# Kernel tuning notes

Measured on AMD Instinct MI355X. Metric: run time of the kernel, lower is better.

Reference implementation:

```python
import jax, jax.numpy as jnp
import numpy as np

B, S, D, H = 2, 2048, 1024, 16
HD = D // H

def setup_inputs() -> dict:
    key = jax.random.key(0)
    ks = jax.random.split(key, 7)
    s = 1.0 / np.sqrt(D)
    return {
        "x": jax.random.normal(ks[0], (B, S, D), dtype=jnp.float32),
        "Wq": jax.random.uniform(ks[1], (D, D), jnp.float32, -s, s),
        "bq": jax.random.uniform(ks[2], (D,), jnp.float32, -s, s),
        "Wk": jax.random.uniform(ks[3], (D, D), jnp.float32, -s, s),
        "bk": jax.random.uniform(ks[4], (D,), jnp.float32, -s, s),
        "Wv": jax.random.uniform(ks[5], (D, D), jnp.float32, -s, s),
        "bv": jax.random.uniform(ks[6], (D,), jnp.float32, -s, s),
    }

def reference(x, Wq, bq, Wk, bk, Wv, bv):
    b, s, d = x.shape
    def proj(W, bias):
        # [b,s,d] -> [b,H,s,hd]
        y = x @ W + bias
        return y.reshape(b, s, H, HD).transpose(0, 2, 1, 3)
    Q = proj(Wq, bq)
    K = proj(Wk, bk)
    V = proj(Wv, bv)
    # NOTE: original scales by head_dim**0.5 (not sqrt) -> divide by sqrt(HD)
    scores = jnp.einsum("bhqd,bhkd->bhqk", Q, K) / (HD ** 0.5)
    attn = jax.nn.softmax(scores, axis=-1)
    out = jnp.einsum("bhqk,bhkd->bhqd", attn, V)
    out = out.transpose(0, 2, 1, 3).reshape(b, s, d)
    return out + x
```

## Files before the change

### kernel.cpp

```cpp
#include <hip/hip_runtime.h>
#include <stdint.h>

typedef float f32x4 __attribute__((ext_vector_type(4)));
typedef __bf16 bf16x8 __attribute__((ext_vector_type(8)));

union Frag {
    bf16x8 v;
    uint32_t u[4];
    __bf16 e[8];
    uint4 q;
};

constexpr int B_ = 2, S_ = 2048, D_ = 1024, H_ = 16, HD_ = 64;
constexpr int M_ = B_ * S_;

__host__ __device__ constexpr int kperm(int kl) {
    return ((kl & 12) << 1) | ((kl & 16) >> 2) | (kl & 3);
}

typedef const __attribute__((address_space(1))) char gch_t;
typedef __attribute__((address_space(3))) char lch_t;
#define GLD(g, l) __builtin_amdgcn_global_load_lds((gch_t*)(g), (lch_t*)(l), 16, 0, 0)

#define MFMA16(a, b, c) __builtin_amdgcn_mfma_f32_16x16x32_bf16((a), (b), (c), 0, 0, 0)

#define WAIT5 do { asm volatile("s_waitcnt vmcnt(5)" ::: "memory"); \
                   __builtin_amdgcn_sched_barrier(0); } while (0)
#define WAIT2 do { asm volatile("s_waitcnt vmcnt(2)" ::: "memory"); \
                   __builtin_amdgcn_sched_barrier(0); } while (0)
#define WAIT0 do { asm volatile("s_waitcnt vmcnt(0)" ::: "memory"); \
                   __builtin_amdgcn_sched_barrier(0); } while (0)
#define BARR() __builtin_amdgcn_s_barrier()

__global__ __launch_bounds__(256) void k_prep(
        const float* __restrict__ x, const float* __restrict__ Wq,
        const float* __restrict__ Wk, const float* __restrict__ Wv,
        __bf16* __restrict__ xb, __bf16* __restrict__ Wt) {
    __shared__ float tile[32][33];
    const int tid = threadIdx.x;

    if (blockIdx.x < 512) {
        int t = blockIdx.x * 256 + tid;
        const float4* src = (const float4*)(x + (size_t)t * 32);
        __bf16 buf[32];
#pragma unroll
        for (int j = 0; j < 8; ++j) {
            float4 f = src[j];
            buf[kperm(4 * j + 0)] = (__bf16)f.x;
            buf[kperm(4 * j + 1)] = (__bf16)f.y;
            buf[kperm(4 * j + 2)] = (__bf16)f.z;
            buf[kperm(4 * j + 3)] = (__bf16)f.w;
        }
        uint4* dst = (uint4*)(xb + (size_t)t * 32);
#pragma unroll
        for (int j = 0; j < 4; ++j) dst[j] = ((const uint4*)buf)[j];
        return;
    }

    int pb = blockIdx.x - 512;
    int p = pb >> 10;
    int rem = pb & 1023;
    const float* W = (p == 0) ? Wq : (p == 1 ? Wk : Wv);
    int n0 = (rem & 31) * 32, k0 = (rem >> 5) * 32;
    int tx = tid & 31, ty = tid >> 5;
#pragma unroll
    for (int t = 0; t < 4; ++t)
        tile[ty + 8 * t][tx] = W[(size_t)(k0 + ty + 8 * t) * D_ + n0 + tx];
    __syncthreads();
#pragma unroll
    for (int t = 0; t < 4; ++t)
        Wt[(size_t)(p * D_ + n0 + ty + 8 * t) * D_ + k0 + kperm(tx)] = (__bf16)tile[tx][ty + 8 * t];
}

__global__ __launch_bounds__(512, 4) void k_qkv(
        const __bf16* __restrict__ xb, const __bf16* __restrict__ Wt,
        const float* __restrict__ bq, const float* __restrict__ bk, const float* __restrict__ bv,
        __bf16* __restrict__ Qb, __bf16* __restrict__ Kb, __bf16* __restrict__ Vt) {
    __shared__ __align__(16) char ldsA[2][16384];
    __shared__ __align__(16) char ldsB[2][24576];

    const int tid = threadIdx.x;
    const int lane = tid & 63, wid = tid >> 6;
    const int wr = wid >> 2, wc = wid & 3;
    const int g = lane >> 4, qr = lane & 15, qr7 = qr & 7;
    const int lr = lane >> 3, lp = lane & 7;
    const int c = lp ^ lr;

    int bid = blockIdx.x;
    int xcd = bid & 7, local = bid >> 3;
    int mt = (xcd & 3) * 8 + (local & 7);
    int nt = (xcd >> 2) * 8 + (local >> 3);
    const int m0 = mt * 128, n0 = nt * 192;

    const __bf16* aSrc = xb + (size_t)(m0 + wid * 16 + lr) * D_ + c * 8;
    const __bf16* bSrc = Wt + (size_t)(n0 + wid * 24 + lr) * D_ + c * 8;
    const int dstA = wid * 2048;
    const int dstB = wid * 3072;

    f32x4 acc[4][3] = {};

    auto STAGE = [&](int buf, int kk) {
        GLD(aSrc + kk,           ldsA[buf] + dstA);
        GLD(aSrc + kk + 8 * D_,  ldsA[buf] + dstA + 1024);
        GLD(bSrc + kk,           ldsB[buf] + dstB);
        GLD(bSrc + kk + 8 * D_,  ldsB[buf] + dstB + 1024);
        GLD(bSrc + kk + 16 * D_, ldsB[buf] + dstB + 2048);
    };
    auto COMPUTE = [&](int buf) {
#pragma unroll
        for (int kc = 0; kc < 2; ++kc) {
            Frag afr[4], bfr[3];
#pragma unroll
            for (int mi = 0; mi < 4; ++mi) {
                int r = wr * 64 + mi * 16 + qr;
                afr[mi].q = *(const uint4*)(ldsA[buf] + r * 128 + (((4 * kc + g) ^ qr7) << 4));
            }
#pragma unroll
            for (int ni = 0; ni < 3; ++ni) {
                int r = wc * 48 + ni * 16 + qr;
                bfr[ni].q = *(const uint4*)(ldsB[buf] + r * 128 + (((4 * kc + g) ^ qr7) << 4));
            }
            __builtin_amdgcn_s_setprio(1);
#pragma unroll
            for (int mi = 0; mi < 4; ++mi)
#pragma unroll
                for (int ni = 0; ni < 3; ++ni)
                    acc[mi][ni] = MFMA16(afr[mi].v, bfr[ni].v, acc[mi][ni]);
            __builtin_amdgcn_s_setprio(0);
        }
    };

    STAGE(0, 0);
    STAGE(1, 64);
    for (int t = 0; t < 12; t += 2) {
        WAIT5; BARR(); COMPUTE(0); BARR(); STAGE(0, (t + 2) * 64);
        WAIT5; BARR(); COMPUTE(1); BARR(); STAGE(1, (t + 3) * 64);
    }
    WAIT5; BARR(); COMPUTE(0); BARR(); STAGE(0, 14 * 64);
    WAIT5; BARR(); COMPUTE(1); BARR(); STAGE(1, 15 * 64);
    WAIT5; BARR(); COMPUTE(0);
    WAIT0; BARR(); COMPUTE(1);

#pragma unroll
    for (int ni = 0; ni < 3; ++ni) {
        int n = n0 + wc * 48 + ni * 16 + qr;
        int p = n >> 10;
        int d = n & 1023;
        const float* bias = (p == 0) ? bq : (p == 1 ? bk : bv);
        float bb = bias[d];
        int h = d >> 6, hd = d & 63;
        int hd_s = (hd & 32) | kperm(hd & 31);
#pragma unroll
        for (int mi = 0; mi < 4; ++mi) {
#pragma unroll
            for (int r = 0; r < 4; ++r) {
                int m = m0 + wr * 64 + mi * 16 + 4 * g + r;
                float vv = acc[mi][ni][r] + bb;
                int b = m >> 11, s = m & 2047;
                if (p == 0) {
                    vv *= 0.18033688f;
                    Qb[((size_t)((b * H_ + h) * S_ + s)) * HD_ + hd_s] = (__bf16)vv;
                } else if (p == 1) {
                    Kb[((size_t)((b * H_ + h) * S_ + s)) * HD_ + hd_s] = (__bf16)vv;
                } else {
                    int s_s = (s & ~31) | kperm(s & 31);
                    Vt[((size_t)((b * H_ + h) * HD_ + hd)) * S_ + s_s] = (__bf16)vv;
                }
            }
        }
    }
}

__global__ __launch_bounds__(512) void k_attn(
        const __bf16* __restrict__ Qb, const __bf16* __restrict__ Kb,
        const __bf16* __restrict__ Vt, const float* __restrict__ x,
        float* __restrict__ out) {
    __shared__ __align__(16) char ldsK[2][8192];
    __shared__ __align__(16) char ldsV[2][8192];

    const int tid = threadIdx.x;
    const int lane = tid & 63, w = tid >> 6;
    const int g = lane >> 4, qr = lane & 15, qr7 = qr & 7;
    const int lr = lane >> 3, lp = lane & 7;
    const int c = lp ^ lr;

    int lid = blockIdx.x;
    int xcd = lid & 7, loc = lid >> 3;
    int bh = xcd * 4 + (loc >> 4);
    int q0 = (loc & 15) * 128;
    const int qrow = q0 + w * 16 + qr;

    Frag qf[2];
    const __bf16* qp = Qb + ((size_t)bh * S_ + qrow) * HD_;
    qf[0].q = *(const uint4*)(qp + g * 8);
    qf[1].q = *(const uint4*)(qp + 32 + g * 8);

    const __bf16* kSrc = Kb + ((size_t)bh * S_ + w * 8 + lr) * HD_ + c * 8;
    const __bf16* vSrc = Vt + ((size_t)bh * HD_ + w * 8 + lr) * S_ + c * 8;
    const int dstOff = w * 8 * 128;

    f32x4 oacc[4] = {};
    f32x4 lacc = {};

    Frag ones;
    ones.u[0] = ones.u[1] = ones.u[2] = ones.u[3] = 0x3f803f80u;

    auto STAGE = [&](int buf, int kv0) {
        GLD(kSrc + (size_t)kv0 * HD_, ldsK[buf] + dstOff);
        GLD(vSrc + kv0,               ldsV[buf] + dstOff);
    };

    auto TILE = [&](int buf) {
        f32x4 sc[4];
        __builtin_amdgcn_s_setprio(1);
#pragma unroll
        for (int kt = 0; kt < 4; ++kt) {
            const char* base = ldsK[buf] + (kt * 16 + qr) * 128;
            Frag k0, k1;
            k0.q = *(const uint4*)(base + ((g ^ qr7) << 4));
            k1.q = *(const uint4*)(base + (((4 + g) ^ qr7) << 4));
            f32x4 z = {};
            z = MFMA16(k0.v, qf[0].v, z);
            z = MFMA16(k1.v, qf[1].v, z);
            sc[kt] = z;
        }
        __builtin_amdgcn_s_setprio(0);

        Frag pa[2];
#pragma unroll
        for (int r = 0; r < 4; ++r) {
            pa[0].e[r]     = (__bf16)__builtin_amdgcn_exp2f(sc[0][r]);
            pa[0].e[4 + r] = (__bf16)__builtin_amdgcn_exp2f(sc[1][r]);
            pa[1].e[r]     = (__bf16)__builtin_amdgcn_exp2f(sc[2][r]);
            pa[1].e[4 + r] = (__bf16)__builtin_amdgcn_exp2f(sc[3][r]);
        }

        __builtin_amdgcn_s_setprio(1);
        lacc = MFMA16(pa[0].v, ones.v, lacc);
        lacc = MFMA16(pa[1].v, ones.v, lacc);

#pragma unroll
        for (int ni = 0; ni < 4; ++ni) {
            const char* base = ldsV[buf] + (ni * 16 + qr) * 128;
            Frag v0, v1;
            v0.q = *(const uint4*)(base + ((g ^ qr7) << 4));
            v1.q = *(const uint4*)(base + (((4 + g) ^ qr7) << 4));
            oacc[ni] = MFMA16(pa[0].v, v0.v, oacc[ni]);
            oacc[ni] = MFMA16(pa[1].v, v1.v, oacc[ni]);
        }
        __builtin_amdgcn_s_setprio(0);
    };

    STAGE(0, 0);
    STAGE(1, 64);
    for (int t = 0; t < 28; t += 2) {
        WAIT2; BARR(); TILE(0); BARR(); STAGE(0, (t + 2) * 64);
        WAIT2; BARR(); TILE(1); BARR(); STAGE(1, (t + 3) * 64);
    }
    WAIT2; BARR(); TILE(0); BARR(); STAGE(0, 30 * 64);
    WAIT2; BARR(); TILE(1); BARR(); STAGE(1, 31 * 64);
    WAIT2; BARR(); TILE(0);
    WAIT0; BARR(); TILE(1);

    float rs[4];
#pragma unroll
    for (int r = 0; r < 4; ++r) rs[r] = 1.0f / lacc[r];

    int b = bh >> 4, h = bh & 15;
#pragma unroll
    for (int ni = 0; ni < 4; ++ni) {
#pragma unroll
        for (int r = 0; r < 4; ++r) {
            int q = q0 + w * 16 + 4 * g + r;
            size_t addr = ((size_t)(b * S_ + q)) * D_ + h * 64 + ni * 16 + qr;
            out[addr] = oacc[ni][r] * rs[r] + x[addr];
        }
    }
}

extern "C" void kernel_launch(void* const* d_in, const int* in_sizes, int n_in,
                              void* d_out, int out_size, void* d_ws, size_t ws_size,
                              hipStream_t stream) {
    const float* x  = (const float*)d_in[0];
    const float* Wq = (const float*)d_in[1];
    const float* bq = (const float*)d_in[2];
    const float* Wk = (const float*)d_in[3];
    const float* bk = (const float*)d_in[4];
    const float* Wv = (const float*)d_in[5];
    const float* bv = (const float*)d_in[6];
    float* out = (float*)d_out;

    char* ws = (char*)d_ws;
    __bf16* xb = (__bf16*)(ws);
    __bf16* Wt = (__bf16*)(ws + 8388608);
    __bf16* Qb = (__bf16*)(ws + 14680064);
    __bf16* Kb = (__bf16*)(ws + 23068672);
    __bf16* Vt = (__bf16*)(ws + 31457280);

    k_prep<<<3584, 256, 0, stream>>>(x, Wq, Wk, Wv, xb, Wt);
    k_qkv<<<512, 512, 0, stream>>>(xb, Wt, bq, bk, bv, Qb, Kb, Vt);
    k_attn<<<512, 512, 0, stream>>>(Qb, Kb, Vt, x, out);
}
```

Before: 96.06 us.

## Process two query row-groups per wave in attention with 256-thread blocks

```diff
diff --git a/kernel.cpp b/kernel.cpp
--- a/kernel.cpp
+++ b/kernel.cpp
@@ -26,7 +26,7 @@
 
 #define WAIT5 do { asm volatile("s_waitcnt vmcnt(5)" ::: "memory"); \
                    __builtin_amdgcn_sched_barrier(0); } while (0)
-#define WAIT2 do { asm volatile("s_waitcnt vmcnt(2)" ::: "memory"); \
+#define WAIT4 do { asm volatile("s_waitcnt vmcnt(4)" ::: "memory"); \
                    __builtin_amdgcn_sched_barrier(0); } while (0)
 #define WAIT0 do { asm volatile("s_waitcnt vmcnt(0)" ::: "memory"); \
                    __builtin_amdgcn_sched_barrier(0); } while (0)
@@ -171,7 +171,7 @@
     }
 }
 
-__global__ __launch_bounds__(512) void k_attn(
+__global__ __launch_bounds__(256, 2) void k_attn(
         const __bf16* __restrict__ Qb, const __bf16* __restrict__ Kb,
         const __bf16* __restrict__ Vt, const float* __restrict__ x,
         float* __restrict__ out) {
@@ -188,30 +188,34 @@
     int xcd = lid & 7, loc = lid >> 3;
     int bh = xcd * 4 + (loc >> 4);
     int q0 = (loc & 15) * 128;
-    const int qrow = q0 + w * 16 + qr;
-
-    Frag qf[2];
-    const __bf16* qp = Qb + ((size_t)bh * S_ + qrow) * HD_;
-    qf[0].q = *(const uint4*)(qp + g * 8);
-    qf[1].q = *(const uint4*)(qp + 32 + g * 8);
-
-    const __bf16* kSrc = Kb + ((size_t)bh * S_ + w * 8 + lr) * HD_ + c * 8;
-    const __bf16* vSrc = Vt + ((size_t)bh * HD_ + w * 8 + lr) * S_ + c * 8;
-    const int dstOff = w * 8 * 128;
-
-    f32x4 oacc[4] = {};
-    f32x4 lacc = {};
+
+    Frag qf[2][2];
+#pragma unroll
+    for (int s = 0; s < 2; ++s) {
+        const __bf16* qp = Qb + ((size_t)bh * S_ + q0 + w * 32 + s * 16 + qr) * HD_;
+        qf[s][0].q = *(const uint4*)(qp + g * 8);
+        qf[s][1].q = *(const uint4*)(qp + 32 + g * 8);
+    }
+
+    const __bf16* kSrc = Kb + ((size_t)bh * S_ + w * 16 + lr) * HD_ + c * 8;
+    const __bf16* vSrc = Vt + ((size_t)bh * HD_ + w * 16 + lr) * S_ + c * 8;
+    const int dstOff = w * 2048;
+
+    f32x4 oacc0[4] = {}, oacc1[4] = {};
+    f32x4 lacc0 = {}, lacc1 = {};
 
     Frag ones;
     ones.u[0] = ones.u[1] = ones.u[2] = ones.u[3] = 0x3f803f80u;
 
     auto STAGE = [&](int buf, int kv0) {
-        GLD(kSrc + (size_t)kv0 * HD_, ldsK[buf] + dstOff);
-        GLD(vSrc + kv0,               ldsV[buf] + dstOff);
+        GLD(kSrc + (size_t)kv0 * HD_,           ldsK[buf] + dstOff);
+        GLD(kSrc + (size_t)kv0 * HD_ + 8 * HD_, ldsK[buf] + dstOff + 1024);
+        GLD(vSrc + kv0,                         ldsV[buf] + dstOff);
+        GLD(vSrc + kv0 + 8 * S_,                ldsV[buf] + dstOff + 1024);
     };
 
     auto TILE = [&](int buf) {
-        f32x4 sc[4];
+        f32x4 sc0[4], sc1[4];
         __builtin_amdgcn_s_setprio(1);
 #pragma unroll
         for (int kt = 0; kt < 4; ++kt) {
@@ -219,25 +223,34 @@
             Frag k0, k1;
             k0.q = *(const uint4*)(base + ((g ^ qr7) << 4));
             k1.q = *(const uint4*)(base + (((4 + g) ^ qr7) << 4));
-            f32x4 z = {};
-            z = MFMA16(k0.v, qf[0].v, z);
-            z = MFMA16(k1.v, qf[1].v, z);
-            sc[kt] = z;
+            f32x4 z0 = {}, z1 = {};
+            z0 = MFMA16(k0.v, qf[0][0].v, z0);
+            z0 = MFMA16(k1.v, qf[0][1].v, z0);
+            z1 = MFMA16(k0.v, qf[1][0].v, z1);
+            z1 = MFMA16(k1.v, qf[1][1].v, z1);
+            sc0[kt] = z0;
+            sc1[kt] = z1;
         }
         __builtin_amdgcn_s_setprio(0);
 
-        Frag pa[2];
+        Frag pa0[2], pa1[2];
 #pragma unroll
         for (int r = 0; r < 4; ++r) {
-            pa[0].e[r]     = (__bf16)__builtin_amdgcn_exp2f(sc[0][r]);
-            pa[0].e[4 + r] = (__bf16)__builtin_amdgcn_exp2f(sc[1][r]);
-            pa[1].e[r]     = (__bf16)__builtin_amdgcn_exp2f(sc[2][r]);
-            pa[1].e[4 + r] = (__bf16)__builtin_amdgcn_exp2f(sc[3][r]);
+            pa0[0].e[r]     = (__bf16)__builtin_amdgcn_exp2f(sc0[0][r]);
+            pa0[0].e[4 + r] = (__bf16)__builtin_amdgcn_exp2f(sc0[1][r]);
+            pa0[1].e[r]     = (__bf16)__builtin_amdgcn_exp2f(sc0[2][r]);
+            pa0[1].e[4 + r] = (__bf16)__builtin_amdgcn_exp2f(sc0[3][r]);
+            pa1[0].e[r]     = (__bf16)__builtin_amdgcn_exp2f(sc1[0][r]);
+            pa1[0].e[4 + r] = (__bf16)__builtin_amdgcn_exp2f(sc1[1][r]);
+            pa1[1].e[r]     = (__bf16)__builtin_amdgcn_exp2f(sc1[2][r]);
+            pa1[1].e[4 + r] = (__bf16)__builtin_amdgcn_exp2f(sc1[3][r]);
         }
 
         __builtin_amdgcn_s_setprio(1);
-        lacc = MFMA16(pa[0].v, ones.v, lacc);
-        lacc = MFMA16(pa[1].v, ones.v, lacc);
+        lacc0 = MFMA16(pa0[0].v, ones.v, lacc0);
+        lacc0 = MFMA16(pa0[1].v, ones.v, lacc0);
+        lacc1 = MFMA16(pa1[0].v, ones.v, lacc1);
+        lacc1 = MFMA16(pa1[1].v, ones.v, lacc1);
 
 #pragma unroll
         for (int ni = 0; ni < 4; ++ni) {
@@ -245,8 +258,10 @@
             Frag v0, v1;
             v0.q = *(const uint4*)(base + ((g ^ qr7) << 4));
             v1.q = *(const uint4*)(base + (((4 + g) ^ qr7) << 4));
-            oacc[ni] = MFMA16(pa[0].v, v0.v, oacc[ni]);
-            oacc[ni] = MFMA16(pa[1].v, v1.v, oacc[ni]);
+            oacc0[ni] = MFMA16(pa0[0].v, v0.v, oacc0[ni]);
+            oacc0[ni] = MFMA16(pa0[1].v, v1.v, oacc0[ni]);
+            oacc1[ni] = MFMA16(pa1[0].v, v0.v, oacc1[ni]);
+            oacc1[ni] = MFMA16(pa1[1].v, v1.v, oacc1[ni]);
         }
         __builtin_amdgcn_s_setprio(0);
     };
@@ -254,26 +269,31 @@
     STAGE(0, 0);
     STAGE(1, 64);
     for (int t = 0; t < 28; t += 2) {
-        WAIT2; BARR(); TILE(0); BARR(); STAGE(0, (t + 2) * 64);
-        WAIT2; BARR(); TILE(1); BARR(); STAGE(1, (t + 3) * 64);
-    }
-    WAIT2; BARR(); TILE(0); BARR(); STAGE(0, 30 * 64);
-    WAIT2; BARR(); TILE(1); BARR(); STAGE(1, 31 * 64);
-    WAIT2; BARR(); TILE(0);
+        WAIT4; BARR(); TILE(0); BARR(); STAGE(0, (t + 2) * 64);
+        WAIT4; BARR(); TILE(1); BARR(); STAGE(1, (t + 3) * 64);
+    }
+    WAIT4; BARR(); TILE(0); BARR(); STAGE(0, 30 * 64);
+    WAIT4; BARR(); TILE(1); BARR(); STAGE(1, 31 * 64);
+    WAIT4; BARR(); TILE(0);
     WAIT0; BARR(); TILE(1);
 
-    float rs[4];
-#pragma unroll
-    for (int r = 0; r < 4; ++r) rs[r] = 1.0f / lacc[r];
+    float rs0[4], rs1[4];
+#pragma unroll
+    for (int r = 0; r < 4; ++r) {
+        rs0[r] = 1.0f / lacc0[r];
+        rs1[r] = 1.0f / lacc1[r];
+    }
 
     int b = bh >> 4, h = bh & 15;
 #pragma unroll
     for (int ni = 0; ni < 4; ++ni) {
 #pragma unroll
         for (int r = 0; r < 4; ++r) {
-            int q = q0 + w * 16 + 4 * g + r;
-            size_t addr = ((size_t)(b * S_ + q)) * D_ + h * 64 + ni * 16 + qr;
-            out[addr] = oacc[ni][r] * rs[r] + x[addr];
+            int q0r = q0 + w * 32 + 4 * g + r;
+            size_t a0 = ((size_t)(b * S_ + q0r)) * D_ + h * 64 + ni * 16 + qr;
+            out[a0] = oacc0[ni][r] * rs0[r] + x[a0];
+            size_t a1 = ((size_t)(b * S_ + q0r + 16)) * D_ + h * 64 + ni * 16 + qr;
+            out[a1] = oacc1[ni][r] * rs1[r] + x[a1];
         }
     }
 }
@@ -299,5 +319,5 @@
 
     k_prep<<<3584, 256, 0, stream>>>(x, Wq, Wk, Wv, xb, Wt);
     k_qkv<<<512, 512, 0, stream>>>(xb, Wt, bq, bk, bv, Qb, Kb, Vt);
-    k_attn<<<512, 512, 0, stream>>>(Qb, Kb, Vt, x, out);
-}
+    k_attn<<<512, 256, 0, stream>>>(Qb, Kb, Vt, x, out);
+}
```

New measurement: 95.47 us. Within noise of the previous version (-0.6%).
